# Performance work log

Hardware: AMD Instinct MI355X
Metric: run time of the kernel (lower is better)

The kernel has to match this reference:

```python
import jax, jax.numpy as jnp
import numpy as np
import math

N_EMBD = 1024
NUM_HEADS = 16
EXPANSION = 4
B, S = 2, 2048
EPS = 1e-5


def setup_inputs() -> dict:
    key = jax.random.key(0)
    ks = jax.random.split(key, 8)
    E, H = N_EMBD, NUM_HEADS
    D_FF = E * EXPANSION
    sd = 0.02
    return {
        "x": jax.random.normal(ks[0], (B, S, E), dtype=jnp.float32),
        "w_kqv": jax.random.normal(ks[1], (E, 3 * E), dtype=jnp.float32) * sd,
        "ln1_g": jnp.ones((E,), jnp.float32),
        "ln1_b": jnp.zeros((E,), jnp.float32),
        "ln2_g": jnp.ones((E,), jnp.float32),
        "ln2_b": jnp.zeros((E,), jnp.float32),
        "w1": jax.random.normal(ks[2], (E, D_FF), dtype=jnp.float32) * sd,
        "b1": jnp.zeros((D_FF,), jnp.float32),
        "w2": jax.random.normal(ks[3], (D_FF, E), dtype=jnp.float32) * sd,
        "b2": jnp.zeros((E,), jnp.float32),
    }


def _layernorm(x, g, b):
    mu = jnp.mean(x, axis=-1, keepdims=True)
    var = jnp.mean((x - mu) ** 2, axis=-1, keepdims=True)
    return (x - mu) * jax.lax.rsqrt(var + EPS) * g + b


def _alibi_slopes(num_heads):
    x = (2.0 ** 8) ** (1.0 / num_heads)
    return jnp.asarray([1.0 / x ** (i + 1) for i in range(num_heads)], jnp.float32)


def _attention(x, w_kqv):
    batch, seq, e = x.shape
    H = NUM_HEADS
    d = e // H
    scale = math.sqrt(e)  # note: original scales by sqrt(n_embd), not sqrt(head_dim)
    kqv = x @ w_kqv  # [B,S,3E]; chunk order in source: key, query, value
    k, q, v = jnp.split(kqv, 3, axis=-1)
    k = k.reshape(batch, seq, H, d).transpose(0, 2, 1, 3)  # [B,H,S,d]
    q = q.reshape(batch, seq, H, d).transpose(0, 2, 1, 3)
    v = v.reshape(batch, seq, H, d).transpose(0, 2, 1, 3)
    pos = jnp.arange(seq)
    rel = pos[None, :] - pos[:, None]  # [S,S], (j - i)
    bias = _alibi_slopes(H)[:, None, None] * rel[None, :, :]  # [H,S,S]
    score = jnp.einsum("bhqd,bhkd->bhqk", q, k) / scale + bias[None]
    causal = rel <= 0  # lower triangular
    score = jnp.where(causal[None, None], score, -jnp.inf)
    attn = jax.nn.softmax(score, axis=-1)
    out = jnp.einsum("bhqk,bhkd->bhqd", attn, v)
    return out.transpose(0, 2, 1, 3).reshape(batch, seq, e)


def reference(x, w_kqv, ln1_g, ln1_b, ln2_g, ln2_b, w1, b1, w2, b2):
    x = x + _attention(_layernorm(x, ln1_g, ln1_b), w_kqv)
    h = _layernorm(x, ln2_g, ln2_b)
    ffn = jax.nn.relu(h @ w1 + b1) @ w2 + b2
    return x + ffn
```

## Files before the change

### kernel.cpp

```cpp
#include <hip/hip_runtime.h>

typedef unsigned short u16;
typedef unsigned int u32;

typedef __bf16 bf16x8 __attribute__((ext_vector_type(8)));
typedef float f32x4 __attribute__((ext_vector_type(4)));

static __device__ __forceinline__ float b2f(u16 h) {
  union { u32 u; float f; } c; c.u = ((u32)h) << 16; return c.f;
}
static __device__ __forceinline__ u16 f2b(float f) {
  union { float f; u32 u; } c; c.f = f;
  u32 u = c.u;
  u32 r = (u + 0x7fffu + ((u >> 16) & 1u)) >> 16;
  return (u16)r;
}
static __device__ __forceinline__ bool probe_f32(const u32* p) {
  return p[0] == 0x3F800000u;
}

__global__ __launch_bounds__(256) void ln_kernel(const void* xa, const void* xb,
                                                 const void* g, const void* bta,
                                                 u16* __restrict__ out,
                                                 const u32* __restrict__ probe,
                                                 int ext) {
  bool pf = probe_f32(probe);
  const void* xv = pf ? xb : xa;
  bool rf32 = ext && pf;
  int row = blockIdx.x, tid = threadIdx.x;
  float v0, v1, v2, v3;
  if (rf32) {
    float4 u = ((const float4*)xv)[row * 256 + tid];
    v0 = u.x; v1 = u.y; v2 = u.z; v3 = u.w;
  } else {
    ushort4 u = ((const ushort4*)xv)[row * 256 + tid];
    v0 = b2f(u.x); v1 = b2f(u.y); v2 = b2f(u.z); v3 = b2f(u.w);
  }
  float s = v0 + v1 + v2 + v3;
  float q = v0 * v0 + v1 * v1 + v2 * v2 + v3 * v3;
  for (int off = 32; off > 0; off >>= 1) {
    s += __shfl_down(s, off, 64);
    q += __shfl_down(q, off, 64);
  }
  __shared__ float red[8];
  int wave = tid >> 6, lane = tid & 63;
  if (lane == 0) { red[wave] = s; red[wave + 4] = q; }
  __syncthreads();
  s = red[0] + red[1] + red[2] + red[3];
  q = red[4] + red[5] + red[6] + red[7];
  float mean = s * (1.0f / 1024.0f);
  float var = q * (1.0f / 1024.0f) - mean * mean;
  float rstd = rsqrtf(var + 1e-5f);
  float g0, g1, g2, g3, bb0, bb1, bb2, bb3;
  if (pf) {
    float4 gg = ((const float4*)g)[tid];
    float4 bb = ((const float4*)bta)[tid];
    g0 = gg.x; g1 = gg.y; g2 = gg.z; g3 = gg.w;
    bb0 = bb.x; bb1 = bb.y; bb2 = bb.z; bb3 = bb.w;
  } else {
    ushort4 gg = ((const ushort4*)g)[tid];
    ushort4 bb = ((const ushort4*)bta)[tid];
    g0 = b2f(gg.x); g1 = b2f(gg.y); g2 = b2f(gg.z); g3 = b2f(gg.w);
    bb0 = b2f(bb.x); bb1 = b2f(bb.y); bb2 = b2f(bb.z); bb3 = b2f(bb.w);
  }
  ushort4 o;
  o.x = f2b((v0 - mean) * rstd * g0 + bb0);
  o.y = f2b((v1 - mean) * rstd * g1 + bb1);
  o.z = f2b((v2 - mean) * rstd * g2 + bb2);
  o.w = f2b((v3 - mean) * rstd * g3 + bb3);
  ((ushort4*)(out + (long)row * 1024))[tid] = o;
}

__global__ __launch_bounds__(256) void trans_kernel(const void* __restrict__ in,
                                                    u16* __restrict__ out,
                                                    int K, int N,
                                                    const u32* __restrict__ probe) {
  bool pf = probe_f32(probe);
  __shared__ float T[64 * 65];
  int n0 = blockIdx.x * 64, k0 = blockIdx.y * 64;
  int t = threadIdx.x;
  int kr = t >> 2, nc = (t & 3) * 16;
  if (pf) {
    const float* src = (const float*)in + (long)(k0 + kr) * N + n0 + nc;
#pragma unroll
    for (int j0 = 0; j0 < 16; j0 += 4) {
      float4 v = *(const float4*)(src + j0);
      T[(nc + j0 + 0) * 65 + kr] = v.x;
      T[(nc + j0 + 1) * 65 + kr] = v.y;
      T[(nc + j0 + 2) * 65 + kr] = v.z;
      T[(nc + j0 + 3) * 65 + kr] = v.w;
    }
  } else {
    const u16* src = (const u16*)in + (long)(k0 + kr) * N + n0 + nc;
#pragma unroll
    for (int j0 = 0; j0 < 16; j0 += 8) {
      uint4 raw = *(const uint4*)(src + j0);
      T[(nc + j0 + 0) * 65 + kr] = b2f((u16)(raw.x & 0xffff));
      T[(nc + j0 + 1) * 65 + kr] = b2f((u16)(raw.x >> 16));
      T[(nc + j0 + 2) * 65 + kr] = b2f((u16)(raw.y & 0xffff));
      T[(nc + j0 + 3) * 65 + kr] = b2f((u16)(raw.y >> 16));
      T[(nc + j0 + 4) * 65 + kr] = b2f((u16)(raw.z & 0xffff));
      T[(nc + j0 + 5) * 65 + kr] = b2f((u16)(raw.z >> 16));
      T[(nc + j0 + 6) * 65 + kr] = b2f((u16)(raw.w & 0xffff));
      T[(nc + j0 + 7) * 65 + kr] = b2f((u16)(raw.w >> 16));
    }
  }
  __syncthreads();
  int nr = t >> 2, kc = (t & 3) * 16;
  u16 o[16];
#pragma unroll
  for (int i = 0; i < 16; i++) o[i] = f2b(T[nr * 65 + kc + i]);
  u16* dst = out + (long)(n0 + nr) * K + k0 + kc;
  *(uint4*)dst = *(const uint4*)&o[0];
  *(uint4*)(dst + 8) = *(const uint4*)&o[8];
}

template <int BM, int BK, int BIAS, int RELU, int RES, int EXTOUT, int VSPLIT>
__global__ __launch_bounds__(256) void gemm_bt(const u16* __restrict__ A,
                                               const u16* __restrict__ BT,
                                               void* __restrict__ C,
                                               int M, int N, int K,
                                               const void* __restrict__ bias,
                                               const void* __restrict__ res,
                                               u16* __restrict__ vt,
                                               const u32* __restrict__ probe) {
  bool pf = probe_f32(probe);
  const int WI = BM / 32;
  const int KK = BK / 32;
  const int CPR = BK / 8;
  __shared__ __align__(16) u16 As[BM * BK];
  __shared__ __align__(16) u16 Bs[128 * BK];
  int tid = threadIdx.x;
  int wave = tid >> 6, lane = tid & 63, quad = lane >> 4, lm = lane & 15;

  int nbx = gridDim.x;
  int nwg = nbx * gridDim.y;
  int flat = blockIdx.y * nbx + blockIdx.x;
  int cpx = nwg >> 3;
  int swz = (flat & 7) * cpx + (flat >> 3);
  int bm = swz / nbx, bn = swz % nbx;

  int wm = (wave >> 1) * (BM / 2), wn = (wave & 1) * 64;

  f32x4 acc[WI][4];
  for (int i = 0; i < WI; i++)
    for (int j = 0; j < 4; j++)
      for (int r = 0; r < 4; r++) acc[i][j][r] = 0.0f;

  const u16* Ab = A + (long)(bm * BM) * K;
  const u16* Bb = BT + (long)(bn * 128) * K;

  for (int k0 = 0; k0 < K; k0 += BK) {
#pragma unroll
    for (int p = 0; p < BM * BK / 2048; p++) {
      int c = p * 256 + tid;
      int row = c / CPR;
      int cs = c % CPR;
      int gc = (BK == 64) ? (cs ^ (row & 7)) : cs;
      __builtin_amdgcn_global_load_lds(
          (const __attribute__((address_space(1))) u32*)(Ab + (long)row * K + k0 + gc * 8),
          (__attribute__((address_space(3))) u32*)(&As[p * 2048 + wave * 512]),
          16, 0, 0);
    }
#pragma unroll
    for (int p = 0; p < 128 * BK / 2048; p++) {
      int c = p * 256 + tid;
      int row = c / CPR;
      int cs = c % CPR;
      int gc = (BK == 64) ? (cs ^ (row & 7)) : cs;
      __builtin_amdgcn_global_load_lds(
          (const __attribute__((address_space(1))) u32*)(Bb + (long)row * K + k0 + gc * 8),
          (__attribute__((address_space(3))) u32*)(&Bs[p * 2048 + wave * 512]),
          16, 0, 0);
    }
    __syncthreads();
    bf16x8 af[WI][KK], bfr[4][KK];
    for (int i = 0; i < WI; i++)
      for (int kk = 0; kk < KK; kk++) {
        int slot = (BK == 64) ? ((kk * 4 + quad) ^ (lm & 7)) : quad;
        af[i][kk] = *(const bf16x8*)&As[(wm + i * 16 + lm) * BK + slot * 8];
      }
    for (int j = 0; j < 4; j++)
      for (int kk = 0; kk < KK; kk++) {
        int slot = (BK == 64) ? ((kk * 4 + quad) ^ (lm & 7)) : quad;
        bfr[j][kk] = *(const bf16x8*)&Bs[(wn + j * 16 + lm) * BK + slot * 8];
      }
    for (int kk = 0; kk < KK; kk++)
      for (int i = 0; i < WI; i++)
        for (int j = 0; j < 4; j++)
          acc[i][j] = __builtin_amdgcn_mfma_f32_16x16x32_bf16(af[i][kk], bfr[j][kk],
                                                              acc[i][j], 0, 0, 0);
    __syncthreads();
  }

  for (int j = 0; j < 4; j++) {
    int col = bn * 128 + wn + j * 16 + lm;
    if (VSPLIT && col >= 2048) {
      int hd = col - 2048;
      for (int i = 0; i < WI; i++) {
        int rowi0 = bm * BM + wm + i * 16 + quad * 4;
        int s = rowi0 & 2047, bb = rowi0 >> 11;
        ushort4 o4;
        o4.x = f2b(acc[i][j][0]);
        o4.y = f2b(acc[i][j][1]);
        o4.z = f2b(acc[i][j][2]);
        o4.w = f2b(acc[i][j][3]);
        *(ushort4*)&vt[((long)(bb * 1024 + hd)) * 2048 + s] = o4;
      }
      continue;
    }
    float bv = 0.0f;
    if (BIAS) bv = pf ? ((const float*)bias)[col] : b2f(((const u16*)bias)[col]);
    for (int i = 0; i < WI; i++) {
      for (int r = 0; r < 4; r++) {
        int rowi = bm * BM + wm + i * 16 + quad * 4 + r;
        float v = acc[i][j][r] + bv;
        if (RELU) v = fmaxf(v, 0.0f);
        long idx = (long)rowi * N + col;
        if (RES) v += pf ? ((const float*)res)[idx] : b2f(((const u16*)res)[idx]);
        if (EXTOUT && pf) ((float*)C)[idx] = v;
        else ((u16*)C)[idx] = f2b(v);
      }
    }
  }
}

__global__ __launch_bounds__(256) void attn_kernel(const u16* __restrict__ kqv,
                                                   const u16* __restrict__ vT,
                                                   void* __restrict__ x,
                                                   const u32* __restrict__ probe) {
  bool pf = probe_f32(probe);
  const int S = 2048;
  int tid = threadIdx.x;
  int wave = tid >> 6, lane = tid & 63, quad = lane >> 4, lm = lane & 15;

  int bx = blockIdx.x;
  int bh = bx & 31;
  int qt = 31 - (bx >> 5);
  int b = bh >> 4, h = bh & 15;
  int q0 = qt * 64 + wave * 16;

  __shared__ __align__(16) u16 Ks[2][4096];
  __shared__ __align__(16) u16 Vs[2][4096];
  __shared__ __align__(16) u16 Pw[4][16 * 72];
  u16* P = Pw[wave];

  const float LOG2E = 1.44269504f;
  const float scale2 = 0.03125f * LOG2E;
  const float slope2 = exp2f(-0.5f * (float)(h + 1)) * LOG2E;

  int d0 = tid, rr0 = d0 >> 3, gc0 = (d0 & 7) ^ (rr0 & 7);
  int d1 = 256 + tid, rr1 = d1 >> 3, gc1 = (d1 & 7) ^ (rr1 & 7);
  const u16* kb0 = kqv + (long)(b * S) * 3072 + h * 64;
  const u16* vb0 = vT + (long)(b * 1024 + h * 64) * 2048;

  auto STAGE = [&](int bb, int kt) __attribute__((always_inline)) {
    __builtin_amdgcn_global_load_lds(
        (const __attribute__((address_space(1))) u32*)(kb0 + (long)(kt * 64 + rr0) * 3072 + gc0 * 8),
        (__attribute__((address_space(3))) u32*)(&Ks[bb][wave * 512]), 16, 0, 0);
    __builtin_amdgcn_global_load_lds(
        (const __attribute__((address_space(1))) u32*)(kb0 + (long)(kt * 64 + rr1) * 3072 + gc1 * 8),
        (__attribute__((address_space(3))) u32*)(&Ks[bb][2048 + wave * 512]), 16, 0, 0);
    __builtin_amdgcn_global_load_lds(
        (const __attribute__((address_space(1))) u32*)(vb0 + (long)rr0 * 2048 + kt * 64 + gc0 * 8),
        (__attribute__((address_space(3))) u32*)(&Vs[bb][wave * 512]), 16, 0, 0);
    __builtin_amdgcn_global_load_lds(
        (const __attribute__((address_space(1))) u32*)(vb0 + (long)rr1 * 2048 + kt * 64 + gc1 * 8),
        (__attribute__((address_space(3))) u32*)(&Vs[bb][2048 + wave * 512]), 16, 0, 0);
  };

  bf16x8 aq[2];
  {
    const u16* qp = kqv + (long)(b * S + q0 + lm) * 3072 + 1024 + h * 64 + quad * 8;
    aq[0] = *(const bf16x8*)qp;
    aq[1] = *(const bf16x8*)(qp + 32);
  }

  f32x4 O[4];
  float mrow[4], lpart[4];
  for (int t = 0; t < 4; t++)
    for (int r = 0; r < 4; r++) O[t][r] = 0.0f;
  for (int r = 0; r < 4; r++) { mrow[r] = -1e30f; lpart[r] = 0.0f; }

  float sq2[4];
  for (int r = 0; r < 4; r++)
    sq2[r] = slope2 * (float)(q0 + quad * 4 + r);

  int fr_lo = (quad ^ (lm & 7)) * 8 + lm * 64;
  int fr_hi = ((quad + 4) ^ (lm & 7)) * 8 + lm * 64;

  auto tile = [&](int kt, int bb, bool domask) __attribute__((always_inline)) {
    const u16* Kb = Ks[bb];
    const u16* Vb = Vs[bb];
    f32x4 sv[4];
#pragma unroll
    for (int t = 0; t < 4; t++) {
      bf16x8 k0 = *(const bf16x8*)&Kb[t * 1024 + fr_lo];
      bf16x8 k1 = *(const bf16x8*)&Kb[t * 1024 + fr_hi];
      f32x4 s;
      for (int r = 0; r < 4; r++) s[r] = 0.0f;
      s = __builtin_amdgcn_mfma_f32_16x16x32_bf16(aq[0], k0, s, 0, 0, 0);
      s = __builtin_amdgcn_mfma_f32_16x16x32_bf16(aq[1], k1, s, 0, 0, 0);
      sv[t] = s;
    }
    float lmax[4] = {-1e30f, -1e30f, -1e30f, -1e30f};
#pragma unroll
    for (int t = 0; t < 4; t++) {
      int kc = kt * 64 + t * 16 + lm;
      float sk2 = slope2 * (float)kc;
#pragma unroll
      for (int r = 0; r < 4; r++) {
        float v = sv[t][r] * scale2 + (sk2 - sq2[r]);
        if (domask && (kc > q0 + quad * 4 + r)) v = -1e30f;
        sv[t][r] = v;
        lmax[r] = fmaxf(lmax[r], v);
      }
    }
    bool need = false;
#pragma unroll
    for (int r = 0; r < 4; r++) need = need || (lmax[r] > mrow[r] + 11.0f);
    if (__any(need)) {
#pragma unroll
      for (int off = 1; off < 16; off <<= 1)
#pragma unroll
        for (int r = 0; r < 4; r++)
          lmax[r] = fmaxf(lmax[r], __shfl_xor(lmax[r], off, 64));
#pragma unroll
      for (int r = 0; r < 4; r++) {
        float nm = fmaxf(mrow[r], lmax[r]);
        float a = exp2f(mrow[r] - nm);
        mrow[r] = nm;
        lpart[r] *= a;
#pragma unroll
        for (int t = 0; t < 4; t++) O[t][r] *= a;
      }
    }
#pragma unroll
    for (int t = 0; t < 4; t++) {
#pragma unroll
      for (int r = 0; r < 4; r++) {
        float p = exp2f(sv[t][r] - mrow[r]);
        lpart[r] += p;
        int rw = quad * 4 + r;
        int colS = (t * 16 + lm) ^ (((rw >> 1) & 7) << 3);
        P[rw * 72 + colS] = f2b(p);
      }
    }
    bf16x8 pfr[2];
#pragma unroll
    for (int kk = 0; kk < 2; kk++) {
      int colS = (kk * 32 + quad * 8) ^ (((lm >> 1) & 7) << 3);
      pfr[kk] = *(const bf16x8*)&P[lm * 72 + colS];
    }
#pragma unroll
    for (int t = 0; t < 4; t++) {
      bf16x8 v0 = *(const bf16x8*)&Vb[t * 1024 + fr_lo];
      bf16x8 v1 = *(const bf16x8*)&Vb[t * 1024 + fr_hi];
      O[t] = __builtin_amdgcn_mfma_f32_16x16x32_bf16(pfr[0], v0, O[t], 0, 0, 0);
      O[t] = __builtin_amdgcn_mfma_f32_16x16x32_bf16(pfr[1], v1, O[t], 0, 0, 0);
    }
  };

  STAGE(0, qt);
  __syncthreads();
  int cur = 0;
  for (int kt = qt; kt >= 0; --kt) {
    if (kt > 0) STAGE(cur ^ 1, kt - 1);
    tile(kt, cur, kt == qt);
    __syncthreads();
    cur ^= 1;
  }

#pragma unroll
  for (int off = 1; off < 16; off <<= 1)
#pragma unroll
    for (int r = 0; r < 4; r++) lpart[r] += __shfl_xor(lpart[r], off, 64);
  float rinv[4];
#pragma unroll
  for (int r = 0; r < 4; r++) rinv[r] = 1.0f / lpart[r];
#pragma unroll
  for (int t = 0; t < 4; t++) {
#pragma unroll
    for (int r = 0; r < 4; r++) {
      int qr = q0 + quad * 4 + r;
      long idx = (long)(b * S + qr) * 1024 + h * 64 + t * 16 + lm;
      float val = O[t][r] * rinv[r];
      if (pf) {
        float* xp = (float*)x;
        xp[idx] = val + xp[idx];
      } else {
        u16* xp = (u16*)x;
        xp[idx] = f2b(val + b2f(xp[idx]));
      }
    }
  }
}

extern "C" void kernel_launch(void* const* d_in, const int* in_sizes, int n_in,
                              void* d_out, int out_size, void* d_ws, size_t ws_size,
                              hipStream_t stream) {
  void* x           = d_in[0];
  const void* w_kqv = d_in[1];
  const void* ln1_g = d_in[2];
  const void* ln1_b = d_in[3];
  const void* ln2_g = d_in[4];
  const void* ln2_b = d_in[5];
  const void* w1    = d_in[6];
  const void* b1    = d_in[7];
  const void* w2    = d_in[8];
  const void* b2    = d_in[9];
  const u32* probe = (const u32*)ln1_g;

  char* ws = (char*)d_ws;
  const size_t MB = 1024 * 1024;
  u16* wT   = (u16*)ws;
  u16* kqvb = (u16*)(ws + 8 * MB);
  u16* vTb  = (u16*)(ws + 32 * MB);
  u16* f1   = (u16*)(ws + 8 * MB);
  u16* h    = (u16*)d_out;

  trans_kernel<<<dim3(3072 / 64, 1024 / 64), 256, 0, stream>>>(w_kqv, wT, 1024, 3072, probe);
  ln_kernel<<<4096, 256, 0, stream>>>(x, x, ln1_g, ln1_b, h, probe, 1);
  gemm_bt<128, 64, 0, 0, 0, 0, 1><<<dim3(3072 / 128, 4096 / 128), 256, 0, stream>>>(
      h, wT, kqvb, 4096, 3072, 1024, nullptr, nullptr, vTb, probe);
  attn_kernel<<<dim3(1024), 256, 0, stream>>>(kqvb, vTb, x, probe);
  trans_kernel<<<dim3(4096 / 64, 1024 / 64), 256, 0, stream>>>(w1, wT, 1024, 4096, probe);
  ln_kernel<<<4096, 256, 0, stream>>>(x, x, ln2_g, ln2_b, h, probe, 1);
  gemm_bt<128, 64, 1, 1, 0, 0, 0><<<dim3(4096 / 128, 4096 / 128), 256, 0, stream>>>(
      h, wT, f1, 4096, 4096, 1024, b1, nullptr, nullptr, probe);
  trans_kernel<<<dim3(1024 / 64, 4096 / 64), 256, 0, stream>>>(w2, wT, 4096, 1024, probe);
  gemm_bt<64, 64, 1, 0, 1, 1, 0><<<dim3(1024 / 128, 4096 / 64), 256, 0, stream>>>(
      f1, wT, d_out, 4096, 1024, 4096, b2, x, nullptr, probe);
}
```

Before: 341.1 us.

## Add 256x256 8-wave GEMM with direct-to-LDS loads for QKV and FFN1

Adds a new GEMM kernel with 256x256 block tiles, 512 threads and 8 waves, each wave computing a 128x64 sub-tile. Tiles are staged with global_load_lds into XOR-swizzled, double-buffered shared memory, and the block index is remapped into XCD-aware groups. The kernel interleaves prefetch with MFMA phases under raised wave priority. It replaces the older 128-tile GEMM for the QKV projection and the first FFN layer, aiming for more reuse per tile and less load latency. The 128 KB of LDS and the large accumulator arrays limit occupancy to one block per CU, and the grids become small (192 and 256 blocks).

After: 328.2 us. 3.8% less time.

```diff
diff --git a/kernel.cpp b/kernel.cpp
--- a/kernel.cpp
+++ b/kernel.cpp
@@ -225,6 +225,138 @@
   }
 }
 
+template <int BIAS, int RELU, int VSPLIT>
+__global__ __launch_bounds__(512) void gemm8(const u16* __restrict__ A,
+                                             const u16* __restrict__ BT,
+                                             void* __restrict__ C,
+                                             int M, int N, int K,
+                                             const void* __restrict__ bias,
+                                             u16* __restrict__ vt,
+                                             const u32* __restrict__ probe) {
+  bool pf = probe_f32(probe);
+  __shared__ __align__(16) u16 As[2][256 * 64];
+  __shared__ __align__(16) u16 Bs[2][256 * 64];
+  int tid = threadIdx.x;
+  int wave = tid >> 6, lane = tid & 63, quad = lane >> 4, lm = lane & 15;
+
+  int nbx = gridDim.x;
+  int nwg = nbx * gridDim.y;
+  int flat = blockIdx.y * nbx + blockIdx.x;
+  int cpx = nwg >> 3;
+  int swz = (flat & 7) * cpx + (flat >> 3);
+  int bm = swz / nbx, bn = swz % nbx;
+
+  int wm = (wave >> 2) * 128, wn = (wave & 3) * 64;
+
+  f32x4 acc[8][4];
+#pragma unroll
+  for (int i = 0; i < 8; i++)
+#pragma unroll
+    for (int j = 0; j < 4; j++)
+      for (int r = 0; r < 4; r++) acc[i][j][r] = 0.0f;
+
+  const u16* Ab = A + (long)(bm * 256) * K;
+  const u16* Bb = BT + (long)(bn * 256) * K;
+
+  int srow[4], sgc[4];
+#pragma unroll
+  for (int p = 0; p < 4; p++) {
+    int c = p * 512 + tid;
+    srow[p] = c >> 3;
+    sgc[p] = (c & 7) ^ (srow[p] & 7);
+  }
+  int dstoff = wave * 512;
+
+#define STAGE_A(bb, k0, p)                                                          \
+  __builtin_amdgcn_global_load_lds(                                                 \
+      (const __attribute__((address_space(1))) u32*)(Ab + (long)srow[p] * K + (k0) + sgc[p] * 8), \
+      (__attribute__((address_space(3))) u32*)(&As[bb][(p) * 4096 + dstoff]), 16, 0, 0)
+#define STAGE_B(bb, k0, p)                                                          \
+  __builtin_amdgcn_global_load_lds(                                                 \
+      (const __attribute__((address_space(1))) u32*)(Bb + (long)srow[p] * K + (k0) + sgc[p] * 8), \
+      (__attribute__((address_space(3))) u32*)(&Bs[bb][(p) * 4096 + dstoff]), 16, 0, 0)
+
+  int NT = K >> 6;
+#pragma unroll
+  for (int p = 0; p < 4; p++) { STAGE_A(0, 0, p); STAGE_B(0, 0, p); }
+  asm volatile("s_waitcnt vmcnt(0)" ::: "memory");
+  __builtin_amdgcn_s_barrier();
+
+  int cur = 0;
+  for (int kt = 0; kt < NT; ++kt) {
+    int k1 = (kt + 1) << 6;
+    bool pre = (kt + 1 < NT);
+    int nb = cur ^ 1;
+#pragma unroll
+    for (int ph = 0; ph < 4; ph++) {
+      const int mh = ph & 1;
+      const int kk = ph >> 1;
+      bf16x8 af[4], bfr[4];
+      int slot = ((kk * 4 + quad) ^ (lm & 7)) * 8;
+#pragma unroll
+      for (int i = 0; i < 4; i++)
+        af[i] = *(const bf16x8*)&As[cur][(wm + mh * 64 + i * 16 + lm) * 64 + slot];
+#pragma unroll
+      for (int j = 0; j < 4; j++)
+        bfr[j] = *(const bf16x8*)&Bs[cur][(wn + j * 16 + lm) * 64 + slot];
+      if (pre) {
+        if (ph == 0) {
+#pragma unroll
+          for (int p = 0; p < 4; p++) STAGE_A(nb, k1, p);
+        } else if (ph == 1) {
+#pragma unroll
+          for (int p = 0; p < 4; p++) STAGE_B(nb, k1, p);
+        }
+      }
+      __builtin_amdgcn_s_barrier();
+      __builtin_amdgcn_s_setprio(1);
+#pragma unroll
+      for (int i = 0; i < 4; i++)
+#pragma unroll
+        for (int j = 0; j < 4; j++)
+          acc[mh * 4 + i][j] = __builtin_amdgcn_mfma_f32_16x16x32_bf16(
+              af[i], bfr[j], acc[mh * 4 + i][j], 0, 0, 0);
+      __builtin_amdgcn_s_setprio(0);
+      if (ph == 3) asm volatile("s_waitcnt vmcnt(0)" ::: "memory");
+      __builtin_amdgcn_s_barrier();
+    }
+    cur ^= 1;
+  }
+#undef STAGE_A
+#undef STAGE_B
+
+#pragma unroll
+  for (int j = 0; j < 4; j++) {
+    int col = bn * 256 + wn + j * 16 + lm;
+    if (VSPLIT && col >= 2048) {
+      int hd = col - 2048;
+#pragma unroll
+      for (int i = 0; i < 8; i++) {
+        int rowi0 = bm * 256 + wm + i * 16 + quad * 4;
+        int s = rowi0 & 2047, bb = rowi0 >> 11;
+        ushort4 o4;
+        o4.x = f2b(acc[i][j][0]);
+        o4.y = f2b(acc[i][j][1]);
+        o4.z = f2b(acc[i][j][2]);
+        o4.w = f2b(acc[i][j][3]);
+        *(ushort4*)&vt[((long)(bb * 1024 + hd)) * 2048 + s] = o4;
+      }
+      continue;
+    }
+    float bv = 0.0f;
+    if (BIAS) bv = pf ? ((const float*)bias)[col] : b2f(((const u16*)bias)[col]);
+#pragma unroll
+    for (int i = 0; i < 8; i++) {
+      for (int r = 0; r < 4; r++) {
+        int rowi = bm * 256 + wm + i * 16 + quad * 4 + r;
+        float v = acc[i][j][r] + bv;
+        if (RELU) v = fmaxf(v, 0.0f);
+        ((u16*)C)[(long)rowi * N + col] = f2b(v);
+      }
+    }
+  }
+}
+
 __global__ __launch_bounds__(256) void attn_kernel(const u16* __restrict__ kqv,
                                                    const u16* __restrict__ vT,
                                                    void* __restrict__ x,
@@ -421,13 +553,13 @@
 
   trans_kernel<<<dim3(3072 / 64, 1024 / 64), 256, 0, stream>>>(w_kqv, wT, 1024, 3072, probe);
   ln_kernel<<<4096, 256, 0, stream>>>(x, x, ln1_g, ln1_b, h, probe, 1);
-  gemm_bt<128, 64, 0, 0, 0, 0, 1><<<dim3(3072 / 128, 4096 / 128), 256, 0, stream>>>(
-      h, wT, kqvb, 4096, 3072, 1024, nullptr, nullptr, vTb, probe);
+  gemm8<0, 0, 1><<<dim3(3072 / 256, 4096 / 256), 512, 0, stream>>>(
+      h, wT, kqvb, 4096, 3072, 1024, nullptr, vTb, probe);
   attn_kernel<<<dim3(1024), 256, 0, stream>>>(kqvb, vTb, x, probe);
   trans_kernel<<<dim3(4096 / 64, 1024 / 64), 256, 0, stream>>>(w1, wT, 1024, 4096, probe);
   ln_kernel<<<4096, 256, 0, stream>>>(x, x, ln2_g, ln2_b, h, probe, 1);
-  gemm_bt<128, 64, 1, 1, 0, 0, 0><<<dim3(4096 / 128, 4096 / 128), 256, 0, stream>>>(
-      h, wT, f1, 4096, 4096, 1024, b1, nullptr, nullptr, probe);
+  gemm8<1, 1, 0><<<dim3(4096 / 256, 4096 / 256), 512, 0, stream>>>(
+      h, wT, f1, 4096, 4096, 1024, b1, nullptr, probe);
   trans_kernel<<<dim3(1024 / 64, 4096 / 64), 256, 0, stream>>>(w2, wT, 4096, 1024, probe);
   gemm_bt<64, 64, 1, 0, 1, 1, 0><<<dim3(1024 / 128, 4096 / 64), 256, 0, stream>>>(
       f1, wT, d_out, 4096, 1024, 4096, b2, x, nullptr, probe);
```
